# Kernel tuning notes

Measured on AMD Instinct MI355X. Metric: run time of the kernel, lower is better.

The kernel has to match this reference:

```python
import jax, jax.numpy as jnp
import numpy as np
import math

B, N = 1, 768
C_S, C_Z, C_H, H, P_QK, P_V = 256, 128, 128, 8, 8, 12
EPS, INF, LN_EPS = 1e-8, 1e5, 1e-5


def _quat_to_rot(q):
    # q: [..., 4] normalized quaternion (w, x, y, z) -> [..., 3, 3]
    w, x, y, z = jnp.moveaxis(q, -1, 0)
    r = jnp.stack([
        1 - 2 * (y * y + z * z), 2 * (x * y - w * z), 2 * (x * z + w * y),
        2 * (x * y + w * z), 1 - 2 * (x * x + z * z), 2 * (y * z - w * x),
        2 * (x * z - w * y), 2 * (y * z + w * x), 1 - 2 * (x * x + y * y),
    ], axis=-1)
    return r.reshape(q.shape[:-1] + (3, 3))


def _ln(x, g, b):
    mu = x.mean(-1, keepdims=True)
    var = ((x - mu) ** 2).mean(-1, keepdims=True)
    return (x - mu) * jax.lax.rsqrt(var + LN_EPS) * g + b


def setup_inputs():
    key = jax.random.key(0)
    ks = jax.random.split(key, 20)
    inp = {}
    inp['s'] = jax.random.normal(ks[0], (B, N, C_S), jnp.float32)
    inp['p'] = jax.random.normal(ks[1], (B, N, N, C_Z), jnp.float32)
    q = jax.random.normal(ks[2], (B, N, 4), jnp.float32)
    inp['rot'] = _quat_to_rot(q / jnp.linalg.norm(q, axis=-1, keepdims=True))
    inp['trans'] = 10.0 * jax.random.normal(ks[3], (B, N, 3), jnp.float32)
    inp['mask'] = jnp.ones((B, N), jnp.float32)
    concat_dim = H * C_H + H * P_V * 4 + H * C_Z
    dims = {'q': (H * C_H, C_S), 'kv': (2 * H * C_H, C_S), 'qp': (H * P_QK * 3, C_S),
            'kvp': (H * (P_QK + P_V) * 3, C_S), 'pb': (H, C_Z), 'o': (C_S, concat_dim),
            't1': (C_S, C_S), 't2': (C_S, C_S), 't3': (C_S, C_S), 'bb': (6, C_S)}
    i = 4
    for nm, (do, di) in dims.items():
        k1, k2 = jax.random.split(ks[i]); i += 1
        inp['W' + nm] = 0.02 * jax.random.normal(k1, (do, di), jnp.float32)
        inp['b' + nm] = 0.02 * jax.random.normal(k2, (do,), jnp.float32)
    inp['head_w'] = 0.1 * jax.random.normal(ks[i], (H,), jnp.float32)
    inp['g1'] = jnp.ones((C_S,), jnp.float32)
    inp['be1'] = jnp.zeros((C_S,), jnp.float32)
    inp['g2'] = jnp.ones((C_S,), jnp.float32)
    inp['be2'] = jnp.zeros((C_S,), jnp.float32)
    return inp


def reference(s, p, rot, trans, mask, Wq, bq, Wkv, bkv, Wqp, bqp, Wkvp, bkvp,
              Wpb, bpb, Wo, bo, Wt1, bt1, Wt2, bt2, Wt3, bt3, Wbb, bbb,
              head_w, g1, be1, g2, be2):
    # ---------------- Invariant Point Attention ----------------
    q = (s @ Wq.T + bq).reshape(B, N, H, C_H)
    kv = (s @ Wkv.T + bkv).reshape(B, N, H, 2 * C_H)
    k, v = kv[..., :C_H], kv[..., C_H:]
    # points: linear output is coordinate-major (x-block, y-block, z-block)
    qp = (s @ Wqp.T + bqp).reshape(B, N, 3, H, P_QK)
    qp = jnp.einsum('bnij,bnjhp->bnhpi', rot, qp) + trans[:, :, None, None, :]
    kvp = (s @ Wkvp.T + bkvp).reshape(B, N, 3, H, P_QK + P_V)
    kvp = jnp.einsum('bnij,bnjhp->bnhpi', rot, kvp) + trans[:, :, None, None, :]
    kp, vp = kvp[..., :P_QK, :], kvp[..., P_QK:, :]
    bias_p = p @ Wpb.T + bpb  # [B,N,N,H]
    a = jnp.einsum('bihc,bjhc->bhij', q, k) * math.sqrt(1.0 / (3 * C_H))
    a = a + math.sqrt(1.0 / 3) * jnp.transpose(bias_p, (0, 3, 1, 2))
    d2 = ((qp[:, :, None] - kp[:, None]) ** 2).sum(-1)  # [B,N,N,H,Pqk]
    hw = jax.nn.softplus(head_w) * math.sqrt(1.0 / (3 * (P_QK * 9.0 / 2)))
    pt_att = -0.5 * (d2 * hw[None, None, None, :, None]).sum(-1)  # [B,N,N,H]
    m2 = mask[:, :, None] * mask[:, None, :]
    a = a + jnp.transpose(pt_att, (0, 3, 1, 2)) + (INF * (m2 - 1.0))[:, None]
    att = jax.nn.softmax(a, axis=-1)  # [B,H,N,N]
    o = jnp.einsum('bhij,bjhc->bihc', att, v).reshape(B, N, H * C_H)
    opt = jnp.einsum('bhij,bjhpx->bihpx', att, vp)  # [B,N,H,Pv,3] global
    opt = jnp.einsum('bnji,bnhpj->bnhpi', rot, opt - trans[:, :, None, None, :])
    opt_norm = jnp.sqrt((opt ** 2).sum(-1) + EPS).reshape(B, N, H * P_V)
    opt_flat = jnp.moveaxis(opt.reshape(B, N, H * P_V, 3), -1, -2).reshape(B, N, 3 * H * P_V)
    opair = jnp.einsum('bhij,bijz->bihz', att, p).reshape(B, N, H * C_Z)
    ipa_out = jnp.concatenate([o, opt_flat, opt_norm, opair], -1) @ Wo.T + bo
    # residual + dropout(eval: identity) + LayerNorm
    s1 = _ln(s + ipa_out, g1, be1)
    # ---------------- StructureTransition (1 layer) ----------------
    x = jax.nn.relu(s1 @ Wt1.T + bt1)
    x = jax.nn.relu(x @ Wt2.T + bt2)
    s2 = _ln(s1 + (x @ Wt3.T + bt3), g2, be2)
    # ---------------- BackboneUpdate + masked quaternion compose ----------------
    upd = (s2 @ Wbb.T + bbb) * mask[..., None]  # [B,N,6]
    qvec = jnp.concatenate([jnp.ones(upd.shape[:-1] + (1,), upd.dtype), upd[..., :3]], -1)
    qvec = qvec / jnp.linalg.norm(qvec, axis=-1, keepdims=True)
    rot_new = jnp.einsum('bnij,bnjk->bnik', rot, _quat_to_rot(qvec))
    trans_new = trans + jnp.einsum('bnij,bnj->bni', rot, upd[..., 3:])
    return (s2, rot_new, trans_new)
```

## Files before the change

kernel.cpp:

```cpp
#include <hip/hip_runtime.h>
#include <hip/hip_bf16.h>
#include <math.h>

#define NN 768
#define CS 256
#define CZ 128
#define CH 128
#define HH 8
#define PQK 8
#define PV 12
#define CONCAT 2432
#define ATT_HSTRIDE (768*768)

typedef __bf16 v8bf __attribute__((ext_vector_type(8)));
typedef __bf16 v4bf __attribute__((ext_vector_type(4)));
typedef float  v4f  __attribute__((ext_vector_type(4)));

__device__ inline unsigned short f2bf(float f) {
    union { float f; unsigned u; } v; v.f = f;
    unsigned r = v.u + 0x7FFFu + ((v.u >> 16) & 1u);
    return (unsigned short)(r >> 16);
}
__device__ inline float bf2f(unsigned short u) {
    union { unsigned u; float f; } v; v.u = ((unsigned)u) << 16; return v.f;
}
__device__ inline unsigned encf(float f) {
    unsigned u = __float_as_uint(f);
    return (u >> 31) ? ~u : (u | 0x80000000u);
}
__device__ inline float decf(unsigned e) {
    unsigned u = (e >> 31) ? (e & 0x7FFFFFFFu) : ~e;
    return __uint_as_float(u);
}

#define NCVT 9
struct CvtDesc {
    const float* src[NCVT];
    unsigned short* dst[NCVT];
    int nelem[NCVT];
    int blk_start[NCVT + 1];
};

__global__ __launch_bounds__(256) void cvt_many(CvtDesc d)
{
    int b = blockIdx.x;
    int seg = 0;
    #pragma unroll
    for (int i = 0; i < NCVT - 1; i++) if (b >= d.blk_start[i + 1]) seg = i + 1;
    int local = b - d.blk_start[seg];
    int base = local * 2048 + threadIdx.x;
    const float* s = d.src[seg];
    unsigned short* o = d.dst[seg];
    int n = d.nelem[seg];
    #pragma unroll
    for (int r = 0; r < 8; r++) {
        int idx = base + r * 256;
        if (idx < n) o[idx] = f2bf(s[idx]);
    }
}

struct ProjDesc {
    const unsigned short* W[4];
    const float* bias[4];
    unsigned short* dstb[4];
    float* dstf[4];
    int D[4];
    int ldc[4];
    int mode[4];
    int blk_start[5];
};

__global__ __launch_bounds__(256) void proj_all(const unsigned short* __restrict__ A, ProjDesc d)
{
    __shared__ unsigned short As[64][40];
    __shared__ unsigned short Ws[64][40];
    int bx = blockIdx.x;
    int seg = 0;
    #pragma unroll
    for (int q = 0; q < 3; q++) if (bx >= d.blk_start[q + 1]) seg = q + 1;
    int bd = (bx - d.blk_start[seg]) * 64;
    int bi = blockIdx.y * 64;
    const unsigned short* W = d.W[seg];
    int D = d.D[seg], ldc = d.ldc[seg];

    int tid = threadIdx.x, lane = tid & 63, wid = tid >> 6;
    int wr = (wid >> 1) * 32, wc = (wid & 1) * 32;
    v4f acc[2][2] = {};
    int lrow = tid >> 2, lcol = (tid & 3) * 8;
    const unsigned short* Ap = A + (size_t)(bi + lrow) * 256 + lcol;
    const unsigned short* Wp = W + (size_t)(bd + lrow) * 256 + lcol;
    bool wv = (bd + lrow) < D;
    int fr = lane & 15, fc = (lane >> 4) * 8;

    for (int k0 = 0; k0 < 256; k0 += 32) {
        *(int4*)&As[lrow][lcol] = *(const int4*)(Ap + k0);
        int4 wz = {0, 0, 0, 0};
        *(int4*)&Ws[lrow][lcol] = wv ? *(const int4*)(Wp + k0) : wz;
        __syncthreads();
        v8bf a0 = *(const v8bf*)&As[wr + fr][fc];
        v8bf a1 = *(const v8bf*)&As[wr + 16 + fr][fc];
        v8bf b0 = *(const v8bf*)&Ws[wc + fr][fc];
        v8bf b1 = *(const v8bf*)&Ws[wc + 16 + fr][fc];
        acc[0][0] = __builtin_amdgcn_mfma_f32_16x16x32_bf16(a0, b0, acc[0][0], 0, 0, 0);
        acc[0][1] = __builtin_amdgcn_mfma_f32_16x16x32_bf16(a0, b1, acc[0][1], 0, 0, 0);
        acc[1][0] = __builtin_amdgcn_mfma_f32_16x16x32_bf16(a1, b0, acc[1][0], 0, 0, 0);
        acc[1][1] = __builtin_amdgcn_mfma_f32_16x16x32_bf16(a1, b1, acc[1][1], 0, 0, 0);
        __syncthreads();
    }
    const float* bias = d.bias[seg];
    int mode = d.mode[seg];
    unsigned short* Cb = d.dstb[seg];
    float* Cf = d.dstf[seg];
    int mrow = (lane >> 4) * 4;
    #pragma unroll
    for (int mi = 0; mi < 2; mi++) {
        #pragma unroll
        for (int ni = 0; ni < 2; ni++) {
            int dd = bd + wc + ni * 16 + fr;
            if (dd < D) {
                #pragma unroll
                for (int r = 0; r < 4; r++) {
                    int m = bi + wr + mi * 16 + mrow + r;
                    float v = acc[mi][ni][r] + bias[dd];
                    if (mode == 2) Cb[(size_t)m * ldc + dd] = f2bf(v);
                    else           Cf[(size_t)m * ldc + dd] = v;
                }
            }
        }
    }
}

template<int SPLITK, int MODE, int RELU>
__global__ __launch_bounds__(256) void mfma_gemm(
    const unsigned short* __restrict__ A,
    const unsigned short* __restrict__ W,
    const float* __restrict__ bias,
    float* __restrict__ C,
    unsigned short* __restrict__ Cb,
    int D, int K, int ldc)
{
    __shared__ unsigned short As[64][40];
    __shared__ unsigned short Ws[64][40];
    int tid = threadIdx.x;
    int bi = blockIdx.y * 64;
    int bd = blockIdx.x * 64;
    int kpb = K / SPLITK;
    int k0b = blockIdx.z * kpb;
    int lane = tid & 63;
    int wid = tid >> 6;
    int wr = (wid >> 1) * 32, wc = (wid & 1) * 32;
    v4f acc[2][2] = {};
    int lrow = tid >> 2;
    int lcol = (tid & 3) * 8;
    const unsigned short* Ap = A + (size_t)(bi + lrow) * K + lcol;
    const unsigned short* Wp = W + (size_t)(bd + lrow) * K + lcol;
    bool wv = (bd + lrow) < D;
    int fr = lane & 15, fc = (lane >> 4) * 8;

    for (int k0 = k0b; k0 < k0b + kpb; k0 += 32) {
        *(int4*)&As[lrow][lcol] = *(const int4*)(Ap + k0);
        int4 wz = {0, 0, 0, 0};
        *(int4*)&Ws[lrow][lcol] = wv ? *(const int4*)(Wp + k0) : wz;
        __syncthreads();
        v8bf a0 = *(const v8bf*)&As[wr + fr][fc];
        v8bf a1 = *(const v8bf*)&As[wr + 16 + fr][fc];
        v8bf b0 = *(const v8bf*)&Ws[wc + fr][fc];
        v8bf b1 = *(const v8bf*)&Ws[wc + 16 + fr][fc];
        acc[0][0] = __builtin_amdgcn_mfma_f32_16x16x32_bf16(a0, b0, acc[0][0], 0, 0, 0);
        acc[0][1] = __builtin_amdgcn_mfma_f32_16x16x32_bf16(a0, b1, acc[0][1], 0, 0, 0);
        acc[1][0] = __builtin_amdgcn_mfma_f32_16x16x32_bf16(a1, b0, acc[1][0], 0, 0, 0);
        acc[1][1] = __builtin_amdgcn_mfma_f32_16x16x32_bf16(a1, b1, acc[1][1], 0, 0, 0);
        __syncthreads();
    }
    int mrow = (lane >> 4) * 4;
    #pragma unroll
    for (int mi = 0; mi < 2; mi++) {
        #pragma unroll
        for (int ni = 0; ni < 2; ni++) {
            int d = bd + wc + ni * 16 + fr;
            if (d < D) {
                #pragma unroll
                for (int r = 0; r < 4; r++) {
                    int m = bi + wr + mi * 16 + mrow + r;
                    float v = acc[mi][ni][r];
                    if (SPLITK > 1) {
                        atomicAdd(&C[(size_t)m * ldc + d], v);
                    } else {
                        v += bias[d];
                        if (RELU) v = fmaxf(v, 0.f);
                        if (MODE != 2) C[(size_t)m * ldc + d] = v;
                        if (MODE >= 1) Cb[(size_t)m * ldc + d] = f2bf(v);
                    }
                }
            }
        }
    }
}

__global__ __launch_bounds__(256) void prep2_kernel(
    const float* __restrict__ qpraw, const float* __restrict__ kvpraw,
    const float* __restrict__ rot, const float* __restrict__ trans,
    const unsigned short* __restrict__ kv_bf,
    unsigned short* __restrict__ qph, unsigned short* __restrict__ qpl,
    unsigned short* __restrict__ kph, unsigned short* __restrict__ kpl,
    unsigned short* __restrict__ Vc)
{
    __shared__ unsigned short tile[32][136];
    int bx = blockIdx.x;
    int t = threadIdx.x;
    if (bx < 672) {
        int id = bx*256 + t;
        int i = id / (HH*28);
        int rem = id % (HH*28);
        int h = rem / 28;
        int idx = rem % 28;
        const float* R = rot + i*9;
        const float* T = trans + i*3;
        float s0, s1, s2;
        if (idx < 8) {
            s0 = qpraw[i*192 +   0 + h*8 + idx];
            s1 = qpraw[i*192 +  64 + h*8 + idx];
            s2 = qpraw[i*192 + 128 + h*8 + idx];
        } else {
            int pp = idx - 8;
            s0 = kvpraw[i*480 +   0 + h*20 + pp];
            s1 = kvpraw[i*480 + 160 + h*20 + pp];
            s2 = kvpraw[i*480 + 320 + h*20 + pp];
        }
        float ov[3];
        ov[0] = R[0]*s0 + R[1]*s1 + R[2]*s2 + T[0];
        ov[1] = R[3]*s0 + R[4]*s1 + R[5]*s2 + T[1];
        ov[2] = R[6]*s0 + R[7]*s1 + R[8]*s2 + T[2];
        if (idx < 8) {
            #pragma unroll
            for (int x = 0; x < 3; x++) {
                unsigned short hi = f2bf(ov[x]);
                qph[i*256 + h*32 + idx*3 + x] = hi;
                qpl[i*256 + h*32 + idx*3 + x] = f2bf(ov[x] - bf2f(hi));
            }
            if (idx == 0) {
                #pragma unroll
                for (int m = 24; m < 32; m++) { qph[i*256+h*32+m] = 0; qpl[i*256+h*32+m] = 0; }
            }
        } else if (idx < 16) {
            int pp = idx - 8;
            #pragma unroll
// ... 95 lines not shown

    __syncthreads();
    v4f aqk[2][2] = {};
    #pragma unroll
    for (int ks = 0; ks < 4; ks++) {
        v8bf a0 = *(const v8bf*)&Qs[wr + fr][ks*32 + fc];
        v8bf a1 = *(const v8bf*)&Qs[wr + 16 + fr][ks*32 + fc];
        v8bf b0 = *(const v8bf*)&Ks[wc + fr][ks*32 + fc];
        v8bf b1 = *(const v8bf*)&Ks[wc + 16 + fr][ks*32 + fc];
        aqk[0][0] = __builtin_amdgcn_mfma_f32_16x16x32_bf16(a0, b0, aqk[0][0], 0, 0, 0);
        aqk[0][1] = __builtin_amdgcn_mfma_f32_16x16x32_bf16(a0, b1, aqk[0][1], 0, 0, 0);
        aqk[1][0] = __builtin_amdgcn_mfma_f32_16x16x32_bf16(a1, b0, aqk[1][0], 0, 0, 0);
        aqk[1][1] = __builtin_amdgcn_mfma_f32_16x16x32_bf16(a1, b1, aqk[1][1], 0, 0, 0);
    }
    float hx = head_w[h];
    float sp = (hx > 20.f) ? hx : log1pf(__expf(hx));
    float hw = sp * 0.09622504486493764f;
    const float scale_qk = 0.05103103630798288f;
    int mrow = (lane >> 4) * 4;
    float val[2][2][4];
    #pragma unroll
    for (int mi = 0; mi < 2; mi++) {
        #pragma unroll
        for (int rr = 0; rr < 4; rr++) {
            float qss = __shfl((mi == 0) ? q2a : q2b, mrow + rr);
            #pragma unroll
            for (int ni = 0; ni < 2; ni++) {
                int jl = wc + ni*16 + fr;
                int il = wr + mi*16 + mrow + rr;
                float kss = (ni == 0) ? k2a : k2b;
                float v = aqk[mi][ni][rr]*scale_qk + hw*ap[mi][ni][rr]
                        - 0.5f*hw*(qss + kss)
                        + 100000.0f*(Mi[il]*Mj[jl] - 1.0f);
                val[mi][ni][rr] = v;
                att[(size_t)h*ATT_HSTRIDE + (size_t)(i0 + il)*768 + (j0 + jl)] = v;
            }
        }
    }
    #pragma unroll
    for (int mi = 0; mi < 2; mi++) {
        #pragma unroll
        for (int rr = 0; rr < 4; rr++) {
            float m = fmaxf(val[mi][0][rr], val[mi][1][rr]);
            #pragma unroll
            for (int d2 = 1; d2 < 16; d2 <<= 1) m = fmaxf(m, __shfl_xor(m, d2));
            if (fr == 0) {
                int il = wr + mi*16 + mrow + rr;
                atomicMax(&m0enc[h*768 + i0 + il], encf(m));
            }
        }
    }
}

__global__ __launch_bounds__(256) void fused_p3s_kernel(
    const float* __restrict__ att0,
    const float* __restrict__ p,
    const float* __restrict__ Wpb, const float* __restrict__ bpb,
    const unsigned* __restrict__ m0enc,
    unsigned short* __restrict__ att_bf,
    float* __restrict__ lpart,
    float* __restrict__ opart)
{
    __shared__ unsigned short ptile[2][64][132];
    __shared__ unsigned short wt[16][72];
    __shared__ float bpb_s[8], m8[8], lsum_w[4][8];

    int i = blockIdx.x;
    int half = blockIdx.y;
    int jbase = half * 384;
    int tid = threadIdx.x, lane = tid & 63, wid = tid >> 6;
    int fr = lane & 15, fc = (lane >> 4) * 8;
    int mrow = (lane >> 4) * 4;

    for (int idx = tid; idx < 16*72; idx += 256) ((unsigned short*)wt)[idx] = 0;
    if (tid < 8) {
        bpb_s[tid] = bpb[tid];
        m8[tid] = decf(m0enc[tid*768 + i]);
    }

    v8bf aW[4];
    #pragma unroll
    for (int ks = 0; ks < 4; ks++) {
        v8bf v = {};
        if (fr < 8) {
            const float* wp = Wpb + fr*128 + ks*32 + fc;
            float4 w0 = *(const float4*)wp;
            float4 w1 = *(const float4*)(wp + 4);
            v[0] = (__bf16)w0.x; v[1] = (__bf16)w0.y; v[2] = (__bf16)w0.z; v[3] = (__bf16)w0.w;
            v[4] = (__bf16)w1.x; v[5] = (__bf16)w1.y; v[6] = (__bf16)w1.z; v[7] = (__bf16)w1.w;
        }
        aW[ks] = v;
    }

    const float* pbase = p + (size_t)i*98304 + (size_t)jbase*128;
    int ldrow = tid >> 4, ldz = (tid & 15) * 8;
    float4 pfA[4], pfB[4];
    #pragma unroll
    for (int r2 = 0; r2 < 4; r2++) {
        const float* src = pbase + (size_t)(r2*16 + ldrow)*128 + ldz;
        pfA[r2] = *(const float4*)src;
        pfB[r2] = *(const float4*)(src + 4);
    }
    #pragma unroll
    for (int r2 = 0; r2 < 4; r2++) {
        v4bf lo, hi;
        lo[0] = (__bf16)pfA[r2].x; lo[1] = (__bf16)pfA[r2].y;
        lo[2] = (__bf16)pfA[r2].z; lo[3] = (__bf16)pfA[r2].w;
        hi[0] = (__bf16)pfB[r2].x; hi[1] = (__bf16)pfB[r2].y;
        hi[2] = (__bf16)pfB[r2].z; hi[3] = (__bf16)pfB[r2].w;
        *(v4bf*)&ptile[0][r2*16 + ldrow][ldz]     = lo;
        *(v4bf*)&ptile[0][r2*16 + ldrow][ldz + 4] = hi;
    }
    #pragma unroll
    for (int r2 = 0; r2 < 4; r2++) {
        const float* src = pbase + (size_t)(64 + r2*16 + ldrow)*128 + ldz;
        pfA[r2] = *(const float4*)src;
        pfB[r2] = *(const float4*)(src + 4);
    }
    __syncthreads();
    float m0l[4];
    #pragma unroll
    for (int r2 = 0; r2 < 4; r2++) m0l[r2] = (mrow == 0) ? m8[r2] : m8[4 + r2];

    v4f accD[2] = {};
    float lacc[4] = {0.f, 0.f, 0.f, 0.f};
    const float sqrt13 = 0.57735026918962576f;
    bool expo = (mrow < 8);

    for (int t64 = 0; t64 < 6; t64++) {
        int cur = t64 & 1;
        int j0 = jbase + t64 * 64;

        v4f bd = {};
        #pragma unroll
        for (int ks = 0; ks < 4; ks++) {
            int c = ks*32 + fc;
            v4bf blo = *(const v4bf*)&ptile[cur][16*wid + fr][c];
            v4bf bhi = *(const v4bf*)&ptile[cur][16*wid + fr][c + 4];
            v8bf b;
            b[0]=blo[0]; b[1]=blo[1]; b[2]=blo[2]; b[3]=blo[3];
            b[4]=bhi[0]; b[5]=bhi[1]; b[6]=bhi[2]; b[7]=bhi[3];
            bd = __builtin_amdgcn_mfma_f32_16x16x32_bf16(aW[ks], b, bd, 0, 0, 0);
        }
        if (expo) {
            int j = 16*wid + fr;
            float a0v[4], w8[4];
            #pragma unroll
            for (int r2 = 0; r2 < 4; r2++)
                a0v[r2] = att0[((size_t)(mrow + r2)*768 + i)*768 + j0 + j];
            #pragma unroll
            for (int r2 = 0; r2 < 4; r2++) {
                int h = mrow + r2;
                float L = a0v[r2] + sqrt13*(bd[r2] + bpb_s[h]);
                w8[r2] = __expf(fminf(L - m0l[r2], 60.f));
            }
            #pragma unroll
            for (int r2 = 0; r2 < 4; r2++) {
                int h = mrow + r2;
                unsigned short wb = f2bf(w8[r2]);
                wt[h][j] = wb;
                att_bf[((size_t)h*768 + i)*768 + j0 + j] = wb;
            }
            #pragma unroll
            for (int m = 1; m < 16; m <<= 1) {
                #pragma unroll
                for (int r2 = 0; r2 < 4; r2++) w8[r2] += __shfl_xor(w8[r2], m);
            }
            #pragma unroll
            for (int r2 = 0; r2 < 4; r2++) lacc[r2] += w8[r2];
        }
        if (t64 < 5) {
            #pragma unroll
            for (int r2 = 0; r2 < 4; r2++) {
                v4bf lo, hi;
                lo[0] = (__bf16)pfA[r2].x; lo[1] = (__bf16)pfA[r2].y;
                lo[2] = (__bf16)pfA[r2].z; lo[3] = (__bf16)pfA[r2].w;
                hi[0] = (__bf16)pfB[r2].x; hi[1] = (__bf16)pfB[r2].y;
                hi[2] = (__bf16)pfB[r2].z; hi[3] = (__bf16)pfB[r2].w;
                *(v4bf*)&ptile[cur ^ 1][r2*16 + ldrow][ldz]     = lo;
                *(v4bf*)&ptile[cur ^ 1][r2*16 + ldrow][ldz + 4] = hi;
            }
            if (t64 < 4) {
                #pragma unroll
                for (int r2 = 0; r2 < 4; r2++) {
                    const float* src = pbase + (size_t)((t64+2)*64 + r2*16 + ldrow)*128 + ldz;
                    pfA[r2] = *(const float4*)src;
                    pfB[r2] = *(const float4*)(src + 4);
                }
            }
        }
        __syncthreads();

        #pragma unroll
        for (int mm = 0; mm < 2; mm++) {
            int zcol = (2*wid + mm)*16 + fr;
            #pragma unroll
            for (int ks = 0; ks < 2; ks++) {
                v8bf b;
                #pragma unroll
                for (int kk = 0; kk < 8; kk++)
                    b[kk] = *(const __bf16*)&ptile[cur][ks*32 + fc + kk][zcol];
                v8bf a = *(const v8bf*)&wt[fr][ks*32 + fc];
                accD[mm] = __builtin_amdgcn_mfma_f32_16x16x32_bf16(a, b, accD[mm], 0, 0, 0);
            }
        }
        __syncthreads();
    }

    if (fr == 0 && expo) {
        #pragma unroll
        for (int r2 = 0; r2 < 4; r2++) lsum_w[wid][mrow + r2] = lacc[r2];
    }
    __syncthreads();
    if (tid < 8) {
        lpart[(size_t)(half*8 + tid)*768 + i] =
            lsum_w[0][tid] + lsum_w[1][tid] + lsum_w[2][tid] + lsum_w[3][tid];
    }
    if (expo) {
        float* ob = opart + (size_t)(half*768 + i)*1024;
        #pragma unroll
        for (int mm = 0; mm < 2; mm++) {
            int z = (2*wid + mm)*16 + fr;
            #pragma unroll
            for (int r2 = 0; r2 < 4; r2++)
                ob[(mrow + r2)*128 + z] = accD[mm][r2];
        }
    }
}

__global__ __launch_bounds__(256) void preduce_kernel(
    const float* __restrict__ lpart, const float* __restrict__ opart,
    float* __restrict__ linv, unsigned short* __restrict__ concat)
{
    __shared__ float inv_s[8];
    int i = blockIdx.x, t = threadIdx.x;
    if (t < 8) {
        float l = lpart[(size_t)t*768 + i] + lpart[(size_t)(8 + t)*768 + i];
        float iv = 1.0f / l;
        inv_s[t] = iv;
        linv[(size_t)t*768 + i] = iv;
    }
    __syncthreads();
    const float* o0 = opart + (size_t)i*1024;
    const float* o1 = opart + (size_t)(768 + i)*1024;
    #pragma unroll
    for (int k = 0; k < 4; k++) {
        int c = t + k*256;
        float s = o0[c] + o1[c];
        concat[(size_t)i*CONCAT + 1408 + c] = f2bf(s * inv_s[c >> 7]);
    }
}

__global__ __launch_bounds__(256) void attvc_mfma(
    const unsigned short* __restrict__ att_bf, const unsigned short* __restrict__ Vc,
    const float* __restrict__ linv, const float* __restrict__ rot,
    const float* __restrict__ trans, unsigned short* __restrict__ concat)
{
    __shared__ unsigned short As[64][72];
    __shared__ unsigned short Bs[64][72];
    int h = blockIdx.z;
    int i0 = blockIdx.y * 64, nd0 = blockIdx.x * 64;
    int tid = threadIdx.x, lane = tid & 63, wid = tid >> 6;
    int wr = (wid >> 1) * 32, wc = (wid & 1) * 32;
    int r = tid >> 2, c8 = (tid & 3) * 16;
    int fr = lane & 15, fc = (lane >> 4) * 8;
    v4f acc[2][2] = {};
    for (int k0 = 0; k0 < 768; k0 += 64) {
        const unsigned short* ag = att_bf + ((size_t)h*768 + i0 + r)*768 + k0 + c8;
        const unsigned short* bg = Vc + ((size_t)h*192 + nd0 + r)*768 + k0 + c8;
        *(int4*)&As[r][c8]     = *(const int4*)ag;
        *(int4*)&As[r][c8 + 8] = *(const int4*)(ag + 8);
        *(int4*)&Bs[r][c8]     = *(const int4*)bg;
        *(int4*)&Bs[r][c8 + 8] = *(const int4*)(bg + 8);
        __syncthreads();
        #pragma unroll
        for (int ks = 0; ks < 2; ks++) {
            v8bf a0 = *(const v8bf*)&As[wr + fr][ks*32 + fc];
            v8bf a1 = *(const v8bf*)&As[wr + 16 + fr][ks*32 + fc];
            v8bf b0 = *(const v8bf*)&Bs[wc + fr][ks*32 + fc];
            v8bf b1 = *(const v8bf*)&Bs[wc + 16 + fr][ks*32 + fc];
            acc[0][0] = __builtin_amdgcn_mfma_f32_16x16x32_bf16(a0, b0, acc[0][0], 0, 0, 0);
            acc[0][1] = __builtin_amdgcn_mfma_f32_16x16x32_bf16(a0, b1, acc[0][1], 0, 0, 0);
            acc[1][0] = __builtin_amdgcn_mfma_f32_16x16x32_bf16(a1, b0, acc[1][0], 0, 0, 0);
            acc[1][1] = __builtin_amdgcn_mfma_f32_16x16x32_bf16(a1, b1, acc[1][1], 0, 0, 0);
        }
        __syncthreads();
    }
    int mrow = (lane >> 4) * 4;
    float lv[2][4];
    #pragma unroll
    for (int mi = 0; mi < 2; mi++) {
        int ibase = i0 + wr + mi*16 + mrow;
        float4 l4 = *(const float4*)&linv[(size_t)h*768 + ibase];
        lv[mi][0] = l4.x; lv[mi][1] = l4.y; lv[mi][2] = l4.z; lv[mi][3] = l4.w;
    }
    if (nd0 < 128) {
        #pragma unroll
        for (int mi = 0; mi < 2; mi++) {
            #pragma unroll
            for (int ni = 0; ni < 2; ni++) {
                int d = nd0 + wc + ni*16 + fr;
                #pragma unroll
                for (int rr = 0; rr < 4; rr++) {
                    int i = i0 + wr + mi*16 + mrow + rr;
                    concat[(size_t)i*CONCAT + h*128 + d] = f2bf(acc[mi][ni][rr] * lv[mi][rr]);
                }
            }
        }
    } else {
        float* opt_s = (float*)&As[0][0];
        #pragma unroll
        for (int mi = 0; mi < 2; mi++) {
            #pragma unroll
            for (int ni = 0; ni < 2; ni++) {
                int c = wc + ni*16 + fr;
                if (c < 36) {
                    #pragma unroll
                    for (int rr = 0; rr < 4; rr++) {
                        int rl = wr + mi*16 + mrow + rr;
                        opt_s[rl*36 + c] = acc[mi][ni][rr] * lv[mi][rr];
                    }
                }
            }
        }
        __syncthreads();
        for (int it = tid; it < 768; it += 256) {
            int rl = it / 12, pp = it % 12;
            int i = i0 + rl;
            const float* R = rot + i*9;
            const float* T = trans + i*3;
            float y0 = opt_s[rl*36 + pp*3 + 0] - T[0];
            float y1 = opt_s[rl*36 + pp*3 + 1] - T[1];
            float y2 = opt_s[rl*36 + pp*3 + 2] - T[2];
            float o0 = R[0]*y0 + R[3]*y1 + R[6]*y2;
            float o1 = R[1]*y0 + R[4]*y1 + R[7]*y2;
            float o2 = R[2]*y0 + R[5]*y1 + R[8]*y2;
            float nrm = sqrtf(o0*o0 + o1*o1 + o2*o2 + 1e-8f);
            int hp = h*12 + pp;
            unsigned short* cb = concat + (size_t)i*CONCAT;
            cb[1024 +   0 + hp] = f2bf(o0);
            cb[1024 +  96 + hp] = f2bf(o1);
            cb[1024 + 192 + hp] = f2bf(o2);
            cb[1312 + hp] = f2bf(nrm);
        }
    }
}

__global__ __launch_bounds__(256) void tail_kernel(
    const float* __restrict__ s, const float* __restrict__ ipa,
    const float* __restrict__ bo,
    const float* __restrict__ g1, const float* __restrict__ be1,
    const unsigned short* __restrict__ Wt1, const float* __restrict__ bt1,
    const unsigned short* __restrict__ Wt2, const float* __restrict__ bt2,
    const unsigned short* __restrict__ Wt3, const float* __restrict__ bt3,
    const float* __restrict__ g2, const float* __restrict__ be2,
    const float* __restrict__ Wbb, const float* __restrict__ bbb,
    const float* __restrict__ mask,
    const float* __restrict__ rot, const float* __restrict__ trans,
    float* __restrict__ out, float* __restrict__ rot_out, float* __restrict__ trans_out)
{
    __shared__ float s1f[32][257];
    __shared__ unsigned short Ab[32][264];
    __shared__ float upd_s[32][6];
    int i0 = blockIdx.x * 32;
    int tid = threadIdx.x, lane = tid & 63, wid = tid >> 6;
    int fr = lane & 15, fc = (lane >> 4) * 8, mrow = (lane >> 4) * 4;

    int r = tid >> 3, cg = (tid & 7) * 32;
    {
        float xv[32];
        float sum = 0.f, sq = 0.f;
        #pragma unroll
        for (int q = 0; q < 8; q++) {
            float4 a = *(const float4*)&s[(size_t)(i0 + r)*256 + cg + q*4];
            float4 b = *(const float4*)&ipa[(size_t)(i0 + r)*256 + cg + q*4];
            float4 c = *(const float4*)&bo[cg + q*4];
            float v0 = a.x + b.x + c.x, v1 = a.y + b.y + c.y;
            float v2 = a.z + b.z + c.z, v3 = a.w + b.w + c.w;
            xv[q*4+0] = v0; xv[q*4+1] = v1; xv[q*4+2] = v2; xv[q*4+3] = v3;
            sum += v0 + v1 + v2 + v3;
            sq  += v0*v0 + v1*v1 + v2*v2 + v3*v3;
        }
        #pragma unroll
        for (int d = 1; d < 8; d <<= 1) { sum += __shfl_xor(sum, d); sq += __shfl_xor(sq, d); }
        float mu = sum * (1.0f/256.0f);
        float var = sq * (1.0f/256.0f) - mu*mu;
        float rsig = 1.0f / sqrtf(var + 1e-5f);
        #pragma unroll
        for (int c = 0; c < 32; c++) {
            float o = (xv[c] - mu) * rsig * g1[cg + c] + be1[cg + c];
            s1f[r][cg + c] = o;
            Ab[r][cg + c] = f2bf(o);
        }
    }
    __syncthreads();

    const unsigned short* Ws[3] = {Wt1, Wt2, Wt3};
    const float* Bs[3] = {bt1, bt2, bt3};
    #pragma unroll
    for (int stage = 0; stage < 3; stage++) {
        const unsigned short* W = Ws[stage];
        const float* bias = Bs[stage];
        v4f acc[2][4] = {};
        #pragma unroll
        for (int k0 = 0; k0 < 8; k0++) {
            v8bf a0 = *(const v8bf*)&Ab[fr][k0*32 + fc];
            v8bf a1 = *(const v8bf*)&Ab[16 + fr][k0*32 + fc];
            #pragma unroll
            for (int n = 0; n < 4; n++) {
                int d = wid*64 + n*16 + fr;
                v8bf b = *(const v8bf*)&W[(size_t)d*256 + k0*32 + fc];
                acc[0][n] = __builtin_amdgcn_mfma_f32_16x16x32_bf16(a0, b, acc[0][n], 0, 0, 0);
                acc[1][n] = __builtin_amdgcn_mfma_f32_16x16x32_bf16(a1, b, acc[1][n], 0, 0, 0);
            }
        }
        __syncthreads();
        if (stage < 2) {
            #pragma unroll
            for (int mi = 0; mi < 2; mi++) {
                #pragma unroll
                for (int n = 0; n < 4; n++) {
                    int d = wid*64 + n*16 + fr;
                    #pragma unroll
                    for (int rr = 0; rr < 4; rr++) {
                        int m = mi*16 + mrow + rr;
                        Ab[m][d] = f2bf(fmaxf(acc[mi][n][rr] + bias[d], 0.f));
                    }
                }
            }
        } else {
            #pragma unroll
            for (int mi = 0; mi < 2; mi++) {
                #pragma unroll
                for (int n = 0; n < 4; n++) {
                    int d = wid*64 + n*16 + fr;
                    #pragma unroll
                    for (int rr = 0; rr < 4; rr++) {
                        int m = mi*16 + mrow + rr;
                        s1f[m][d] += acc[mi][n][rr] + bias[d];
                    }
                }
            }
        }
        __syncthreads();
    }

    {
        float xv[32];
        float sum = 0.f, sq = 0.f;
        #pragma unroll
        for (int c = 0; c < 32; c++) {
            float v = s1f[r][cg + c];
            xv[c] = v; sum += v; sq += v*v;
        }
        #pragma unroll
        for (int d = 1; d < 8; d <<= 1) { sum += __shfl_xor(sum, d); sq += __shfl_xor(sq, d); }
        float mu = sum * (1.0f/256.0f);
        float var = sq * (1.0f/256.0f) - mu*mu;
        float rsig = 1.0f / sqrtf(var + 1e-5f);
        float o4[32];
        #pragma unroll
        for (int c = 0; c < 32; c++)
            o4[c] = (xv[c] - mu) * rsig * g2[cg + c] + be2[cg + c];
        #pragma unroll
// ... 40 lines not shown
            trans_out[i*3 + a] = trans[i*3 + a] + Ri[a*3+0]*t0 + Ri[a*3+1]*t1 + Ri[a*3+2]*t2;
        }
    }
}

extern "C" void kernel_launch(void* const* d_in, const int* in_sizes, int n_in,
                              void* d_out, int out_size, void* d_ws, size_t ws_size,
                              hipStream_t stream)
{
    const float* s      = (const float*)d_in[0];
    const float* p      = (const float*)d_in[1];
    const float* rot    = (const float*)d_in[2];
    const float* trans  = (const float*)d_in[3];
    const float* mask   = (const float*)d_in[4];
    const float* Wq     = (const float*)d_in[5];
    const float* bq     = (const float*)d_in[6];
    const float* Wkv    = (const float*)d_in[7];
    const float* bkv    = (const float*)d_in[8];
    const float* Wqp    = (const float*)d_in[9];
    const float* bqp    = (const float*)d_in[10];
    const float* Wkvp   = (const float*)d_in[11];
    const float* bkvp   = (const float*)d_in[12];
    const float* Wpb    = (const float*)d_in[13];
    const float* bpb    = (const float*)d_in[14];
    const float* Wo     = (const float*)d_in[15];
    const float* bo     = (const float*)d_in[16];
    const float* Wt1    = (const float*)d_in[17];
    const float* bt1    = (const float*)d_in[18];
    const float* Wt2    = (const float*)d_in[19];
    const float* bt2    = (const float*)d_in[20];
    const float* Wt3    = (const float*)d_in[21];
    const float* bt3    = (const float*)d_in[22];
    const float* Wbb    = (const float*)d_in[23];
    const float* bbb    = (const float*)d_in[24];
    const float* head_w = (const float*)d_in[25];
    const float* g1     = (const float*)d_in[26];
    const float* be1    = (const float*)d_in[27];
    const float* g2     = (const float*)d_in[28];
    const float* be2    = (const float*)d_in[29];

    float* out = (float*)d_out;
    char*  wsb = (char*)d_ws;

    size_t off = 0;
    auto alloc = [&](size_t bytes) -> char* {
        char* ptr = wsb + off;
        off += (bytes + 255) & ~(size_t)255;
        return ptr;
    };
    float* qpraw   = (float*)alloc((size_t)NN*192*4);
    float* kvpraw  = (float*)alloc((size_t)NN*480*4);
    float* att     = (float*)alloc((size_t)8*768*768*4);
    float* ipa     = (float*)alloc((size_t)NN*256*4);
    float* linv    = (float*)alloc((size_t)8*768*4);
    float* lpart   = (float*)alloc((size_t)16*768*4);
    float* opart   = (float*)alloc((size_t)2*768*1024*4);
    unsigned* m0enc = (unsigned*)alloc((size_t)8*768*4);
    unsigned short* s_bf    = (unsigned short*)alloc((size_t)NN*256*2);
    unsigned short* Wq_bf   = (unsigned short*)alloc((size_t)1024*256*2);
    unsigned short* Wkv_bf  = (unsigned short*)alloc((size_t)2048*256*2);
    unsigned short* Wqp_bf  = (unsigned short*)alloc((size_t)192*256*2);
    unsigned short* Wkvp_bf = (unsigned short*)alloc((size_t)480*256*2);
    unsigned short* Wo_bf   = (unsigned short*)alloc((size_t)256*2432*2);
    unsigned short* Wt1_bf  = (unsigned short*)alloc((size_t)256*256*2);
    unsigned short* Wt2_bf  = (unsigned short*)alloc((size_t)256*256*2);
    unsigned short* Wt3_bf  = (unsigned short*)alloc((size_t)256*256*2);
    unsigned short* q_bf    = (unsigned short*)alloc((size_t)NN*1024*2);
    unsigned short* kv_bf   = (unsigned short*)alloc((size_t)NN*2048*2);
    unsigned short* qph     = (unsigned short*)alloc((size_t)NN*256*2);
    unsigned short* qpl     = (unsigned short*)alloc((size_t)NN*256*2);
    unsigned short* kph     = (unsigned short*)alloc((size_t)NN*256*2);
    unsigned short* kpl     = (unsigned short*)alloc((size_t)NN*256*2);
    unsigned short* Vc      = (unsigned short*)alloc((size_t)8*192*768*2);
    unsigned short* att_bf  = (unsigned short*)alloc((size_t)8*768*768*2);
    unsigned short* concat  = (unsigned short*)alloc((size_t)NN*CONCAT*2);

    hipMemsetAsync(ipa, 0, (size_t)NN*256*4, stream);
    hipMemsetAsync(m0enc, 0, (size_t)8*768*4, stream);

    CvtDesc cd;
    const float* csrc[NCVT]    = {s, Wq, Wkv, Wqp, Wkvp, Wo, Wt1, Wt2, Wt3};
    unsigned short* cdst[NCVT] = {s_bf, Wq_bf, Wkv_bf, Wqp_bf, Wkvp_bf, Wo_bf, Wt1_bf, Wt2_bf, Wt3_bf};
    int csz[NCVT] = {NN*256, 1024*256, 2048*256, 192*256, 480*256, 256*2432, 256*256, 256*256, 256*256};
    int cum = 0;
    for (int i2 = 0; i2 < NCVT; i2++) {
        cd.src[i2] = csrc[i2]; cd.dst[i2] = cdst[i2]; cd.nelem[i2] = csz[i2];
        cd.blk_start[i2] = cum;
        cum += (csz[i2] + 2047) / 2048;
    }
    cd.blk_start[NCVT] = cum;
    cvt_many<<<cum, 256, 0, stream>>>(cd);

    ProjDesc pd;
    pd.W[0] = Wq_bf;   pd.bias[0] = bq;   pd.dstb[0] = q_bf;   pd.dstf[0] = nullptr; pd.D[0] = 1024; pd.ldc[0] = 1024; pd.mode[0] = 2;
    pd.W[1] = Wkv_bf;  pd.bias[1] = bkv;  pd.dstb[1] = kv_bf;  pd.dstf[1] = nullptr; pd.D[1] = 2048; pd.ldc[1] = 2048; pd.mode[1] = 2;
    pd.W[2] = Wqp_bf;  pd.bias[2] = bqp;  pd.dstb[2] = nullptr; pd.dstf[2] = qpraw;  pd.D[2] = 192;  pd.ldc[2] = 192;  pd.mode[2] = 0;
    pd.W[3] = Wkvp_bf; pd.bias[3] = bkvp; pd.dstb[3] = nullptr; pd.dstf[3] = kvpraw; pd.D[3] = 480;  pd.ldc[3] = 480;  pd.mode[3] = 0;
    pd.blk_start[0] = 0; pd.blk_start[1] = 16; pd.blk_start[2] = 48; pd.blk_start[3] = 51; pd.blk_start[4] = 59;
    proj_all<<<dim3(59, 12), 256, 0, stream>>>(s_bf, pd);

    prep2_kernel<<<672 + 192, 256, 0, stream>>>(
        qpraw, kvpraw, rot, trans, kv_bf, qph, qpl, kph, kpl, Vc);

    logits_mfma<<<dim3(12, 12, 8), 256, 0, stream>>>(
        q_bf, kv_bf, qph, qpl, kph, kpl, mask, head_w, att, m0enc);

    fused_p3s_kernel<<<dim3(768, 2), 256, 0, stream>>>(
        att, p, Wpb, bpb, m0enc, att_bf, lpart, opart);
    preduce_kernel<<<768, 256, 0, stream>>>(lpart, opart, linv, concat);

    attvc_mfma<<<dim3(3, 12, 8), 256, 0, stream>>>(att_bf, Vc, linv, rot, trans, concat);

    mfma_gemm<4,0,0><<<dim3(4,12,4), 256, 0, stream>>>(concat, Wo_bf, nullptr, ipa, nullptr, 256, 2432, 256);

    tail_kernel<<<24, 256, 0, stream>>>(
        s, ipa, bo, g1, be1, Wt1_bf, bt1, Wt2_bf, bt2, Wt3_bf, bt3,
        g2, be2, Wbb, bbb, mask, rot, trans,
        out, out + (size_t)NN*256, out + (size_t)NN*256 + (size_t)NN*9);
}
```

Measured before the change: 187.0 us.

## Fuse bf16 conversion into GEMM loads, split pair pass into quarters, merge reduce kernel

Removes the standalone fp32-to-bf16 conversion kernel and converts s and the weights on the fly inside the projection, Wo and tail GEMM loaders. The pair-bias/softmax pass now splits each row into four j-quarters instead of two, for more blocks and parallelism. The separate partial-reduce kernel is folded into extra blocks of the attention-value kernel, which also recomputes the inverse row sums from the partials. This cuts two launches and the intermediate bf16 traffic, at the cost of redundant conversions, repeated fp32 weight reads and larger partial buffers.

```diff
diff --git a/kernel.cpp b/kernel.cpp
--- a/kernel.cpp
+++ b/kernel.cpp
@@ -32,35 +32,17 @@
     unsigned u = (e >> 31) ? (e & 0x7FFFFFFFu) : ~e;
     return __uint_as_float(u);
 }
-
-#define NCVT 9
-struct CvtDesc {
-    const float* src[NCVT];
-    unsigned short* dst[NCVT];
-    int nelem[NCVT];
-    int blk_start[NCVT + 1];
-};
-
-__global__ __launch_bounds__(256) void cvt_many(CvtDesc d)
-{
-    int b = blockIdx.x;
-    int seg = 0;
-    #pragma unroll
-    for (int i = 0; i < NCVT - 1; i++) if (b >= d.blk_start[i + 1]) seg = i + 1;
-    int local = b - d.blk_start[seg];
-    int base = local * 2048 + threadIdx.x;
-    const float* s = d.src[seg];
-    unsigned short* o = d.dst[seg];
-    int n = d.nelem[seg];
-    #pragma unroll
-    for (int r = 0; r < 8; r++) {
-        int idx = base + r * 256;
-        if (idx < n) o[idx] = f2bf(s[idx]);
-    }
+__device__ inline v8bf cvt8(const float* p) {
+    float4 a = *(const float4*)p;
+    float4 b = *(const float4*)(p + 4);
+    v8bf v;
+    v[0] = (__bf16)a.x; v[1] = (__bf16)a.y; v[2] = (__bf16)a.z; v[3] = (__bf16)a.w;
+    v[4] = (__bf16)b.x; v[5] = (__bf16)b.y; v[6] = (__bf16)b.z; v[7] = (__bf16)b.w;
+    return v;
 }
 
 struct ProjDesc {
-    const unsigned short* W[4];
+    const float* W[4];
     const float* bias[4];
     unsigned short* dstb[4];
     float* dstf[4];
@@ -70,7 +52,7 @@
     int blk_start[5];
 };
 
-__global__ __launch_bounds__(256) void proj_all(const unsigned short* __restrict__ A, ProjDesc d)
+__global__ __launch_bounds__(256) void proj_all(const float* __restrict__ S, ProjDesc d)
 {
     __shared__ unsigned short As[64][40];
     __shared__ unsigned short Ws[64][40];
@@ -80,22 +62,22 @@
     for (int q = 0; q < 3; q++) if (bx >= d.blk_start[q + 1]) seg = q + 1;
     int bd = (bx - d.blk_start[seg]) * 64;
     int bi = blockIdx.y * 64;
-    const unsigned short* W = d.W[seg];
+    const float* W = d.W[seg];
     int D = d.D[seg], ldc = d.ldc[seg];
 
     int tid = threadIdx.x, lane = tid & 63, wid = tid >> 6;
     int wr = (wid >> 1) * 32, wc = (wid & 1) * 32;
     v4f acc[2][2] = {};
     int lrow = tid >> 2, lcol = (tid & 3) * 8;
-    const unsigned short* Ap = A + (size_t)(bi + lrow) * 256 + lcol;
-    const unsigned short* Wp = W + (size_t)(bd + lrow) * 256 + lcol;
+    const float* Ap = S + (size_t)(bi + lrow) * 256 + lcol;
+    const float* Wp = W + (size_t)(bd + lrow) * 256 + lcol;
     bool wv = (bd + lrow) < D;
     int fr = lane & 15, fc = (lane >> 4) * 8;
 
     for (int k0 = 0; k0 < 256; k0 += 32) {
-        *(int4*)&As[lrow][lcol] = *(const int4*)(Ap + k0);
-        int4 wz = {0, 0, 0, 0};
-        *(int4*)&Ws[lrow][lcol] = wv ? *(const int4*)(Wp + k0) : wz;
+        *(v8bf*)&As[lrow][lcol] = cvt8(Ap + k0);
+        v8bf wz = {};
+        *(v8bf*)&Ws[lrow][lcol] = wv ? cvt8(Wp + k0) : wz;
         __syncthreads();
         v8bf a0 = *(const v8bf*)&As[wr + fr][fc];
         v8bf a1 = *(const v8bf*)&As[wr + 16 + fr][fc];
@@ -130,21 +112,18 @@
     }
 }
 
-template<int SPLITK, int MODE, int RELU>
-__global__ __launch_bounds__(256) void mfma_gemm(
+__global__ __launch_bounds__(256) void wo_gemm(
     const unsigned short* __restrict__ A,
-    const unsigned short* __restrict__ W,
-    const float* __restrict__ bias,
-    float* __restrict__ C,
-    unsigned short* __restrict__ Cb,
-    int D, int K, int ldc)
+    const float* __restrict__ W,
+    float* __restrict__ C)
 {
     __shared__ unsigned short As[64][40];
     __shared__ unsigned short Ws[64][40];
+    const int K = 2432, D = 256, ldc = 256;
     int tid = threadIdx.x;
     int bi = blockIdx.y * 64;
     int bd = blockIdx.x * 64;
-    int kpb = K / SPLITK;
+    int kpb = K / 4;
     int k0b = blockIdx.z * kpb;
     int lane = tid & 63;
     int wid = tid >> 6;
@@ -153,14 +132,12 @@
     int lrow = tid >> 2;
     int lcol = (tid & 3) * 8;
     const unsigned short* Ap = A + (size_t)(bi + lrow) * K + lcol;
-    const unsigned short* Wp = W + (size_t)(bd + lrow) * K + lcol;
-    bool wv = (bd + lrow) < D;
+    const float* Wp = W + (size_t)(bd + lrow) * K + lcol;
     int fr = lane & 15, fc = (lane >> 4) * 8;
 
     for (int k0 = k0b; k0 < k0b + kpb; k0 += 32) {
         *(int4*)&As[lrow][lcol] = *(const int4*)(Ap + k0);
-        int4 wz = {0, 0, 0, 0};
-        *(int4*)&Ws[lrow][lcol] = wv ? *(const int4*)(Wp + k0) : wz;
+        *(v8bf*)&Ws[lrow][lcol] = cvt8(Wp + k0);
         __syncthreads();
         v8bf a0 = *(const v8bf*)&As[wr + fr][fc];
         v8bf a1 = *(const v8bf*)&As[wr + 16 + fr][fc];
@@ -178,20 +155,10 @@
         #pragma unroll
         for (int ni = 0; ni < 2; ni++) {
             int d = bd + wc + ni * 16 + fr;
-            if (d < D) {
-                #pragma unroll
-                for (int r = 0; r < 4; r++) {
-                    int m = bi + wr + mi * 16 + mrow + r;
-                    float v = acc[mi][ni][r];
-                    if (SPLITK > 1) {
-                        atomicAdd(&C[(size_t)m * ldc + d], v);
-                    } else {
-                        v += bias[d];
-                        if (RELU) v = fmaxf(v, 0.f);
-                        if (MODE != 2) C[(size_t)m * ldc + d] = v;
-                        if (MODE >= 1) Cb[(size_t)m * ldc + d] = f2bf(v);
-                    }
-                }
+            #pragma unroll
+            for (int r = 0; r < 4; r++) {
+                int m = bi + wr + mi * 16 + mrow + r;
+                atomicAdd(&C[(size_t)m * ldc + d], acc[mi][ni][r]);
             }
         }
     }
@@ -393,7 +360,7 @@
     }
 }
 
-__global__ __launch_bounds__(256) void fused_p3s_kernel(
+__global__ __launch_bounds__(256) void fused_p4_kernel(
     const float* __restrict__ att0,
     const float* __restrict__ p,
     const float* __restrict__ Wpb, const float* __restrict__ bpb,
@@ -407,8 +374,8 @@
     __shared__ float bpb_s[8], m8[8], lsum_w[4][8];
 
     int i = blockIdx.x;
-    int half = blockIdx.y;
-    int jbase = half * 384;
+    int quarter = blockIdx.y;
+    int jbase = quarter * 192;
     int tid = threadIdx.x, lane = tid & 63, wid = tid >> 6;
     int fr = lane & 15, fc = (lane >> 4) * 8;
     int mrow = (lane >> 4) * 4;
@@ -423,13 +390,7 @@
     #pragma unroll
     for (int ks = 0; ks < 4; ks++) {
         v8bf v = {};
-        if (fr < 8) {
-            const float* wp = Wpb + fr*128 + ks*32 + fc;
-            float4 w0 = *(const float4*)wp;
-            float4 w1 = *(const float4*)(wp + 4);
-            v[0] = (__bf16)w0.x; v[1] = (__bf16)w0.y; v[2] = (__bf16)w0.z; v[3] = (__bf16)w0.w;
-            v[4] = (__bf16)w1.x; v[5] = (__bf16)w1.y; v[6] = (__bf16)w1.z; v[7] = (__bf16)w1.w;
-        }
+        if (fr < 8) v = cvt8(Wpb + fr*128 + ks*32 + fc);
         aW[ks] = v;
     }
 
@@ -468,7 +429,7 @@
     const float sqrt13 = 0.57735026918962576f;
     bool expo = (mrow < 8);
 
-    for (int t64 = 0; t64 < 6; t64++) {
+    for (int t64 = 0; t64 < 3; t64++) {
         int cur = t64 & 1;
         int j0 = jbase + t64 * 64;
 
@@ -510,7 +471,7 @@
             #pragma unroll
             for (int r2 = 0; r2 < 4; r2++) lacc[r2] += w8[r2];
         }
-        if (t64 < 5) {
+        if (t64 < 2) {
             #pragma unroll
             for (int r2 = 0; r2 < 4; r2++) {
                 v4bf lo, hi;
@@ -521,7 +482,7 @@
                 *(v4bf*)&ptile[cur ^ 1][r2*16 + ldrow][ldz]     = lo;
                 *(v4bf*)&ptile[cur ^ 1][r2*16 + ldrow][ldz + 4] = hi;
             }
-            if (t64 < 4) {
+            if (t64 < 1) {
                 #pragma unroll
                 for (int r2 = 0; r2 < 4; r2++) {
                     const float* src = pbase + (size_t)((t64+2)*64 + r2*16 + ldrow)*128 + ldz;
@@ -554,11 +515,11 @@
     }
     __syncthreads();
     if (tid < 8) {
-        lpart[(size_t)(half*8 + tid)*768 + i] =
+        lpart[(size_t)(quarter*8 + tid)*768 + i] =
             lsum_w[0][tid] + lsum_w[1][tid] + lsum_w[2][tid] + lsum_w[3][tid];
     }
     if (expo) {
-        float* ob = opart + (size_t)(half*768 + i)*1024;
+        float* ob = opart + (size_t)(quarter*768 + i)*1024;
         #pragma unroll
         for (int mm = 0; mm < 2; mm++) {
             int z = (2*wid + mm)*16 + fr;
@@ -569,39 +530,46 @@
     }
 }
 
-__global__ __launch_bounds__(256) void preduce_kernel(
+__global__ __launch_bounds__(256) void attvc2_mfma(
+    const unsigned short* __restrict__ att_bf, const unsigned short* __restrict__ Vc,
     const float* __restrict__ lpart, const float* __restrict__ opart,
-    float* __restrict__ linv, unsigned short* __restrict__ concat)
-{
-    __shared__ float inv_s[8];
-    int i = blockIdx.x, t = threadIdx.x;
-    if (t < 8) {
-        float l = lpart[(size_t)t*768 + i] + lpart[(size_t)(8 + t)*768 + i];
-        float iv = 1.0f / l;
-        inv_s[t] = iv;
-        linv[(size_t)t*768 + i] = iv;
-    }
-    __syncthreads();
-    const float* o0 = opart + (size_t)i*1024;
-    const float* o1 = opart + (size_t)(768 + i)*1024;
-    #pragma unroll
-    for (int k = 0; k < 4; k++) {
-        int c = t + k*256;
-        float s = o0[c] + o1[c];
-        concat[(size_t)i*CONCAT + 1408 + c] = f2bf(s * inv_s[c >> 7]);
-    }
-}
-
-__global__ __launch_bounds__(256) void attvc_mfma(
-    const unsigned short* __restrict__ att_bf, const unsigned short* __restrict__ Vc,
-    const float* __restrict__ linv, const float* __restrict__ rot,
-    const float* __restrict__ trans, unsigned short* __restrict__ concat)
+    const float* __restrict__ rot, const float* __restrict__ trans,
+    unsigned short* __restrict__ concat)
 {
     __shared__ unsigned short As[64][72];
     __shared__ unsigned short Bs[64][72];
     int h = blockIdx.z;
-    int i0 = blockIdx.y * 64, nd0 = blockIdx.x * 64;
+    int i0 = blockIdx.y * 64;
     int tid = threadIdx.x, lane = tid & 63, wid = tid >> 6;
+
+    if (blockIdx.x == 3) {
+        __shared__ float inv_s2[8][8];
+        int t = tid;
+        if (t < 64) {
+            int k = t >> 3, hh = t & 7;
+            int i = i0 + h*8 + k;
+            float l = 0.f;
+            #pragma unroll
+            for (int q = 0; q < 4; q++) l += lpart[(size_t)(q*8 + hh)*768 + i];
+            inv_s2[k][hh] = 1.0f / l;
+        }
+        __syncthreads();
+        #pragma unroll
+        for (int k = 0; k < 8; k++) {
+            int i = i0 + h*8 + k;
+            const float* o0 = opart + (size_t)i*1024;
+            #pragma unroll
+            for (int rep = 0; rep < 4; rep++) {
+                int c = t + rep*256;
+                float s = o0[c] + o0[(size_t)768*1024 + c]
+                        + o0[(size_t)2*768*1024 + c] + o0[(size_t)3*768*1024 + c];
+                concat[(size_t)i*CONCAT + 1408 + c] = f2bf(s * inv_s2[k][c >> 7]);
+            }
+        }
+        return;
+    }
+
+    int nd0 = blockIdx.x * 64;
     int wr = (wid >> 1) * 32, wc = (wid & 1) * 32;
     int r = tid >> 2, c8 = (tid & 3) * 16;
     int fr = lane & 15, fc = (lane >> 4) * 8;
@@ -632,8 +600,13 @@
     #pragma unroll
     for (int mi = 0; mi < 2; mi++) {
         int ibase = i0 + wr + mi*16 + mrow;
-        float4 l4 = *(const float4*)&linv[(size_t)h*768 + ibase];
-        lv[mi][0] = l4.x; lv[mi][1] = l4.y; lv[mi][2] = l4.z; lv[mi][3] = l4.w;
+        #pragma unroll
+        for (int rr = 0; rr < 4; rr++) {
+            float l = 0.f;
+            #pragma unroll
+            for (int q = 0; q < 4; q++) l += lpart[(size_t)(q*8 + h)*768 + ibase + rr];
+            lv[mi][rr] = 1.0f / l;
+        }
     }
     if (nd0 < 128) {
         #pragma unroll
@@ -691,9 +664,9 @@
     const float* __restrict__ s, const float* __restrict__ ipa,
     const float* __restrict__ bo,
     const float* __restrict__ g1, const float* __restrict__ be1,
-    const unsigned short* __restrict__ Wt1, const float* __restrict__ bt1,
-    const unsigned short* __restrict__ Wt2, const float* __restrict__ bt2,
-    const unsigned short* __restrict__ Wt3, const float* __restrict__ bt3,
+    const float* __restrict__ Wt1, const float* __restrict__ bt1,
+    const float* __restrict__ Wt2, const float* __restrict__ bt2,
+    const float* __restrict__ Wt3, const float* __restrict__ bt3,
     const float* __restrict__ g2, const float* __restrict__ be2,
     const float* __restrict__ Wbb, const float* __restrict__ bbb,
     const float* __restrict__ mask,
@@ -736,11 +709,11 @@
     }
     __syncthreads();
 
-    const unsigned short* Ws[3] = {Wt1, Wt2, Wt3};
+    const float* Ws[3] = {Wt1, Wt2, Wt3};
     const float* Bs[3] = {bt1, bt2, bt3};
     #pragma unroll
     for (int stage = 0; stage < 3; stage++) {
-        const unsigned short* W = Ws[stage];
+        const float* W = Ws[stage];
         const float* bias = Bs[stage];
         v4f acc[2][4] = {};
         #pragma unroll
@@ -750,7 +723,7 @@
             #pragma unroll
             for (int n = 0; n < 4; n++) {
                 int d = wid*64 + n*16 + fr;
-                v8bf b = *(const v8bf*)&W[(size_t)d*256 + k0*32 + fc];
+                v8bf b = cvt8(&W[(size_t)d*256 + k0*32 + fc]);
                 acc[0][n] = __builtin_amdgcn_mfma_f32_16x16x32_bf16(a0, b, acc[0][n], 0, 0, 0);
                 acc[1][n] = __builtin_amdgcn_mfma_f32_16x16x32_bf16(a1, b, acc[1][n], 0, 0, 0);
             }
@@ -897,19 +870,9 @@
     float* kvpraw  = (float*)alloc((size_t)NN*480*4);
     float* att     = (float*)alloc((size_t)8*768*768*4);
     float* ipa     = (float*)alloc((size_t)NN*256*4);
-    float* linv    = (float*)alloc((size_t)8*768*4);
-    float* lpart   = (float*)alloc((size_t)16*768*4);
-    float* opart   = (float*)alloc((size_t)2*768*1024*4);
+    float* lpart   = (float*)alloc((size_t)32*768*4);
+    float* opart   = (float*)alloc((size_t)4*768*1024*4);
     unsigned* m0enc = (unsigned*)alloc((size_t)8*768*4);
-    unsigned short* s_bf    = (unsigned short*)alloc((size_t)NN*256*2);
-    unsigned short* Wq_bf   = (unsigned short*)alloc((size_t)1024*256*2);
-    unsigned short* Wkv_bf  = (unsigned short*)alloc((size_t)2048*256*2);
-    unsigned short* Wqp_bf  = (unsigned short*)alloc((size_t)192*256*2);
-    unsigned short* Wkvp_bf = (unsigned short*)alloc((size_t)480*256*2);
-    unsigned short* Wo_bf   = (unsigned short*)alloc((size_t)256*2432*2);
-    unsigned short* Wt1_bf  = (unsigned short*)alloc((size_t)256*256*2);
-    unsigned short* Wt2_bf  = (unsigned short*)alloc((size_t)256*256*2);
-    unsigned short* Wt3_bf  = (unsigned short*)alloc((size_t)256*256*2);
     unsigned short* q_bf    = (unsigned short*)alloc((size_t)NN*1024*2);
     unsigned short* kv_bf   = (unsigned short*)alloc((size_t)NN*2048*2);
     unsigned short* qph     = (unsigned short*)alloc((size_t)NN*256*2);
@@ -923,26 +886,13 @@
     hipMemsetAsync(ipa, 0, (size_t)NN*256*4, stream);
     hipMemsetAsync(m0enc, 0, (size_t)8*768*4, stream);
 
-    CvtDesc cd;
-    const float* csrc[NCVT]    = {s, Wq, Wkv, Wqp, Wkvp, Wo, Wt1, Wt2, Wt3};
-    unsigned short* cdst[NCVT] = {s_bf, Wq_bf, Wkv_bf, Wqp_bf, Wkvp_bf, Wo_bf, Wt1_bf, Wt2_bf, Wt3_bf};
-    int csz[NCVT] = {NN*256, 1024*256, 2048*256, 192*256, 480*256, 256*2432, 256*256, 256*256, 256*256};
-    int cum = 0;
-    for (int i2 = 0; i2 < NCVT; i2++) {
-        cd.src[i2] = csrc[i2]; cd.dst[i2] = cdst[i2]; cd.nelem[i2] = csz[i2];
-        cd.blk_start[i2] = cum;
-        cum += (csz[i2] + 2047) / 2048;
-    }
-    cd.blk_start[NCVT] = cum;
-    cvt_many<<<cum, 256, 0, stream>>>(cd);
-
     ProjDesc pd;
-    pd.W[0] = Wq_bf;   pd.bias[0] = bq;   pd.dstb[0] = q_bf;   pd.dstf[0] = nullptr; pd.D[0] = 1024; pd.ldc[0] = 1024; pd.mode[0] = 2;
-    pd.W[1] = Wkv_bf;  pd.bias[1] = bkv;  pd.dstb[1] = kv_bf;  pd.dstf[1] = nullptr; pd.D[1] = 2048; pd.ldc[1] = 2048; pd.mode[1] = 2;
-    pd.W[2] = Wqp_bf;  pd.bias[2] = bqp;  pd.dstb[2] = nullptr; pd.dstf[2] = qpraw;  pd.D[2] = 192;  pd.ldc[2] = 192;  pd.mode[2] = 0;
-    pd.W[3] = Wkvp_bf; pd.bias[3] = bkvp; pd.dstb[3] = nullptr; pd.dstf[3] = kvpraw; pd.D[3] = 480;  pd.ldc[3] = 480;  pd.mode[3] = 0;
+    pd.W[0] = Wq;   pd.bias[0] = bq;   pd.dstb[0] = q_bf;   pd.dstf[0] = nullptr; pd.D[0] = 1024; pd.ldc[0] = 1024; pd.mode[0] = 2;
+    pd.W[1] = Wkv;  pd.bias[1] = bkv;  pd.dstb[1] = kv_bf;  pd.dstf[1] = nullptr; pd.D[1] = 2048; pd.ldc[1] = 2048; pd.mode[1] = 2;
+    pd.W[2] = Wqp;  pd.bias[2] = bqp;  pd.dstb[2] = nullptr; pd.dstf[2] = qpraw;  pd.D[2] = 192;  pd.ldc[2] = 192;  pd.mode[2] = 0;
+    pd.W[3] = Wkvp; pd.bias[3] = bkvp; pd.dstb[3] = nullptr; pd.dstf[3] = kvpraw; pd.D[3] = 480;  pd.ldc[3] = 480;  pd.mode[3] = 0;
     pd.blk_start[0] = 0; pd.blk_start[1] = 16; pd.blk_start[2] = 48; pd.blk_start[3] = 51; pd.blk_start[4] = 59;
-    proj_all<<<dim3(59, 12), 256, 0, stream>>>(s_bf, pd);
+    proj_all<<<dim3(59, 12), 256, 0, stream>>>(s, pd);
 
     prep2_kernel<<<672 + 192, 256, 0, stream>>>(
         qpraw, kvpraw, rot, trans, kv_bf, qph, qpl, kph, kpl, Vc);
@@ -950,16 +900,16 @@
     logits_mfma<<<dim3(12, 12, 8), 256, 0, stream>>>(
         q_bf, kv_bf, qph, qpl, kph, kpl, mask, head_w, att, m0enc);
 
-    fused_p3s_kernel<<<dim3(768, 2), 256, 0, stream>>>(
+    fused_p4_kernel<<<dim3(768, 4), 256, 0, stream>>>(
         att, p, Wpb, bpb, m0enc, att_bf, lpart, opart);
-    preduce_kernel<<<768, 256, 0, stream>>>(lpart, opart, linv, concat);
-
-    attvc_mfma<<<dim3(3, 12, 8), 256, 0, stream>>>(att_bf, Vc, linv, rot, trans, concat);
-
-    mfma_gemm<4,0,0><<<dim3(4,12,4), 256, 0, stream>>>(concat, Wo_bf, nullptr, ipa, nullptr, 256, 2432, 256);
+
+    attvc2_mfma<<<dim3(4, 12, 8), 256, 0, stream>>>(
+        att_bf, Vc, lpart, opart, rot, trans, concat);
+
+    wo_gemm<<<dim3(4,12,4), 256, 0, stream>>>(concat, Wo, ipa);
 
     tail_kernel<<<24, 256, 0, stream>>>(
-        s, ipa, bo, g1, be1, Wt1_bf, bt1, Wt2_bf, bt2, Wt3_bf, bt3,
+        s, ipa, bo, g1, be1, Wt1, bt1, Wt2, bt2, Wt3, bt3,
         g2, be2, Wbb, bbb, mask, rot, trans,
         out, out + (size_t)NN*256, out + (size_t)NN*256 + (size_t)NN*9);
 }
```

Result: no change. 190.7 us (+2.0%).
